# Kernel tuning notes

Measured on AMD Instinct MI355X. Metric: run time of the kernel, lower is better.

Reference implementation:

```python
import jax, jax.numpy as jnp
import numpy as np

V, E, H, T = 8000, 256, 256, 4  # vocab, embed, lstm hidden, tagset (BMES)
B, S = 64, 512


def setup_inputs() -> dict:
    key = jax.random.key(0)
    ks = jax.random.split(key, 16)
    w = lambda k, shape, s=0.05: (jax.random.normal(k, shape, jnp.float32) * s)
    return {
        "sentence": jax.random.randint(ks[0], (B, S), 0, V),
        "tags": jax.random.randint(ks[1], (B, S), 0, T),
        "length_list": jnp.full((B,), S, dtype=jnp.int32),
        "emb": w(ks[2], (V, E), 0.1),
        "Wih_f": w(ks[3], (4 * H, E)), "Whh_f": w(ks[4], (4 * H, H)), "b_f": jnp.zeros((4 * H,), jnp.float32),
        "Wih_b": w(ks[5], (4 * H, E)), "Whh_b": w(ks[6], (4 * H, H)), "b_b": jnp.zeros((4 * H,), jnp.float32),
        "Wlin": w(ks[7], (T, 2 * H), 0.05), "blin": jnp.zeros((T,), jnp.float32),
        "start_trans": w(ks[8], (T,), 0.1), "end_trans": w(ks[9], (T,), 0.1),
        "transitions": w(ks[10], (T, T), 0.1),
    }


def _lstm_dir(xs, Wih, Whh, b, reverse):
    # xs: [S, B, E] time-major; PyTorch gate order i,f,g,o
    Bv, Hh = xs.shape[1], Whh.shape[1]
    def step(carry, x):
        h, c = carry
        g = x @ Wih.T + h @ Whh.T + b
        i, f, gg, o = jnp.split(g, 4, axis=-1)
        c = jax.nn.sigmoid(f) * c + jax.nn.sigmoid(i) * jnp.tanh(gg)
        h = jax.nn.sigmoid(o) * jnp.tanh(c)
        return (h, c), h
    init = (jnp.zeros((Bv, Hh), xs.dtype), jnp.zeros((Bv, Hh), xs.dtype))
    _, hs = jax.lax.scan(step, init, xs, reverse=reverse)
    return hs  # [S, B, H]


def _crf_llh(emis, tagsT, start, end, trans):
    # emis: [S, B, T] time-major; tagsT: [S, B]. No mask (matches original call).
    e_sc = jnp.take_along_axis(emis, tagsT[:, :, None], axis=2)[..., 0]  # [S, B]
    tr_sc = trans[tagsT[:-1], tagsT[1:]]                                  # [S-1, B]
    num = start[tagsT[0]] + e_sc.sum(0) + tr_sc.sum(0) + end[tagsT[-1]]   # [B]
    alpha = start[None, :] + emis[0]                                      # [B, T]
    def step(alpha, e):
        return jax.nn.logsumexp(alpha[:, :, None] + trans[None], axis=1) + e, None
    alpha, _ = jax.lax.scan(step, alpha, emis[1:])
    denom = jax.nn.logsumexp(alpha + end[None, :], axis=1)                # [B]
    return num - denom


def _viterbi(emis, start, end, trans):
    # emis: [S, B, T] -> best tag path [B, S]
    score = start[None, :] + emis[0]                                      # [B, T]
    def step(score, e):
        cand = score[:, :, None] + trans[None]                            # [B, T_prev, T_next]
        bp = jnp.argmax(cand, axis=1)                                     # [B, T]
        return jnp.max(cand, axis=1) + e, bp
    score, bps = jax.lax.scan(step, score, emis[1:])                      # bps: [S-1, B, T]
    last = jnp.argmax(score + end[None, :], axis=1)                       # [B]
    def back(tag, bp):
        prev = jnp.take_along_axis(bp, tag[:, None], axis=1)[:, 0]
        return prev, prev
    _, path = jax.lax.scan(back, last, bps, reverse=True)                 # [S-1, B]
    return jnp.concatenate([path, last[None]], axis=0).T                  # [B, S]


def reference(sentence, tags, length_list, emb, Wih_f, Whh_f, b_f,
              Wih_b, Whh_b, b_b, Wlin, blin, start_trans, end_trans, transitions):
    xs = jnp.swapaxes(emb[sentence], 0, 1)                                # [S, B, E]
    hf = _lstm_dir(xs, Wih_f, Whh_f, b_f, reverse=False)
    hb = _lstm_dir(xs, Wih_b, Whh_b, b_b, reverse=True)
    h = jnp.concatenate([hf, hb], axis=-1)                                # [S, B, 2H] (dropout = eval identity)
    emis = h @ Wlin.T + blin                                              # [S, B, T]
    loss = -jnp.sum(_crf_llh(emis, tags.T, start_trans, end_trans, transitions))
    tag_seq = _viterbi(emis, start_trans, end_trans, transitions)
    return tag_seq, loss
```

## Files before the change

### kernel.cpp

```cpp
#include <hip/hip_runtime.h>
#include <math.h>

#define Vv 8000
#define Ee 256
#define Hh 256
#define Tt 4
#define Bb 64
#define Ss 512

#define EPROJ_PER_DIR (Vv * 1024)
#define WMAT_PER_DIR  (Ee * 1024)

#define NSTAT 8
#define NSTRM 24
#define STAT_U32 (NSTAT * 512 * 4)

#if defined(__has_builtin)
# if __has_builtin(__builtin_amdgcn_sdot4)
#  define HAS_SDOT4 1
# endif
# if __has_builtin(__builtin_amdgcn_exp2f) && __has_builtin(__builtin_amdgcn_rcpf)
#  define HAS_FASTTRANS 1
# endif
#endif

__device__ __forceinline__ float sigm(float x) { return 1.f / (1.f + expf(-x)); }

__device__ __forceinline__ float sigm_f(float x) {
#ifdef HAS_FASTTRANS
    const float e = __builtin_amdgcn_exp2f(-1.44269504f * x);
    return __builtin_amdgcn_rcpf(1.f + e);
#else
    return 1.f / (1.f + expf(-x));
#endif
}
__device__ __forceinline__ float tanh_f(float x) {
#ifdef HAS_FASTTRANS
    const float e = __builtin_amdgcn_exp2f(-2.88539008f * x);
    return 2.f * __builtin_amdgcn_rcpf(1.f + e) - 1.f;
#else
    return tanhf(x);
#endif
}

__device__ __forceinline__ int dot4i8(unsigned a, unsigned b, int c) {
#ifdef HAS_SDOT4
    return __builtin_amdgcn_sdot4((int)a, (int)b, c, false);
#else
    int s = c;
    #pragma unroll
    for (int i = 0; i < 4; ++i) {
        const int xa = ((int)(a << (24 - 8 * i))) >> 24;
        const int xb = ((int)(b << (24 - 8 * i))) >> 24;
        s += xa * xb;
    }
    return s;
#endif
}

__global__ void prep1_kernel(const float* __restrict__ Wih_f, const float* __restrict__ b_f,
                             const float* __restrict__ Wih_b, const float* __restrict__ b_b,
                             const float* __restrict__ Wlin,
                             float* __restrict__ WihP, float* __restrict__ bP,
                             float* __restrict__ WlinQ)
{
    int tid = blockIdx.x * blockDim.x + threadIdx.x;
    int dir = tid >> 18;
    int r   = tid & 262143;
    int k   = r >> 10;
    int jp  = r & 1023;
    int u   = jp >> 2;
    int g   = jp & 3;
    int row = g * 256 + u;
    const float* Wih = dir ? Wih_b : Wih_f;
    const float* bv  = dir ? b_b   : b_f;
    WihP[dir * WMAT_PER_DIR + k * 1024 + jp] = Wih[row * 256 + k];
    if (r < 1024) {
        bP[dir * 1024 + jp] = bv[row];
        int uu = r >> 2, tt = r & 3;
        WlinQ[(dir * 256 + uu) * 4 + tt] = Wlin[tt * (2 * Hh) + dir * 256 + uu];
    }
}

__global__ __launch_bounds__(256) void scale_kernel(const float* __restrict__ Whh_f,
                                                    const float* __restrict__ Whh_b,
                                                    float* __restrict__ scales)
{
    const int gw = blockIdx.x * 4 + (threadIdx.x >> 6);
    const int lane = threadIdx.x & 63;
    const int dir = gw >> 10;
    const int row = gw & 1023;
    const float* W = dir ? Whh_b : Whh_f;
    const float* src = W + (size_t)row * 256 + lane * 4;
    float m = fmaxf(fmaxf(fabsf(src[0]), fabsf(src[1])),
                    fmaxf(fabsf(src[2]), fabsf(src[3])));
    #pragma unroll
    for (int off = 32; off > 0; off >>= 1) m = fmaxf(m, __shfl_down(m, off));
    if (lane == 0) scales[gw] = fmaxf(m, 1e-12f) / 127.f;
}

__global__ __launch_bounds__(256) void quant_kernel(const float* __restrict__ Whh_f,
                                                    const float* __restrict__ Whh_b,
                                                    const float* __restrict__ scales,
                                                    unsigned int* __restrict__ W8)
{
    const int idx = blockIdx.x * 256 + threadIdx.x;
    const int dir = idx >> 16;
    const int rem = idx & 65535;
    int slot, t, j, kw;
    if (rem < STAT_U32) {
        slot = rem >> 11; const int r2 = rem & 2047; t = r2 >> 2; j = r2 & 3;
        kw = 2 * slot + (j >> 1);
    } else {
        const int q2 = rem - STAT_U32;
        slot = q2 >> 11; const int r2 = q2 & 2047; t = r2 >> 2; j = r2 & 3;
        kw = 2 * NSTAT + 2 * slot + (j >> 1);
    }
    const int rr = j & 1;
    const int u  = t >> 1;
    const int gs = (t & 1) * 2 + rr;
    const int row = gs * 256 + u;
    const float* W = dir ? Whh_b : Whh_f;
    const float sc = scales[dir * 1024 + row];
    const float inv = 1.f / sc;
    unsigned int v = 0;
    #pragma unroll
    for (int i = 0; i < 4; ++i) {
        const float w = W[(size_t)row * 256 + kw * 4 + i];
        int q = (int)rintf(w * inv);
        q = q > 127 ? 127 : (q < -127 ? -127 : q);
        v |= ((unsigned int)(unsigned char)(signed char)q) << (8 * i);
    }
    W8[idx] = v;
}

__global__ __launch_bounds__(512) void wl8_kernel(const float* __restrict__ Wlin,
                                                  unsigned int* __restrict__ wl8T,
                                                  float* __restrict__ scfac)
{
    const int w = threadIdx.x >> 6;
    const int lane = threadIdx.x & 63;
    const int dir = w >> 2, t = w & 3;
    const float4 v = *(const float4*)(Wlin + t * (2 * Hh) + dir * 256 + lane * 4);
    float m = fmaxf(fmaxf(fabsf(v.x), fabsf(v.y)), fmaxf(fabsf(v.z), fabsf(v.w)));
    #pragma unroll
    for (int off = 32; off > 0; off >>= 1) m = fmaxf(m, __shfl_down(m, off));
    const float mall = __builtin_amdgcn_readfirstlane(m);
    const float sc = fmaxf(mall, 1e-12f) / 127.f;
    const float inv = 1.f / sc;
    const float vv[4] = {v.x, v.y, v.z, v.w};
    unsigned int pk = 0;
    #pragma unroll
    for (int i = 0; i < 4; ++i) {
        int q = (int)rintf(vv[i] * inv);
        q = q > 127 ? 127 : (q < -127 ? -127 : q);
        pk |= ((unsigned int)(unsigned char)(signed char)q) << (8 * i);
    }
    wl8T[w * 64 + lane] = pk;
    if (lane == 0) scfac[w] = sc / 127.f;
}

#define BM 64
#define BN 128
#define BK 16
__global__ __launch_bounds__(256) void embproj_gemm(const float* __restrict__ emb,
                                                    const float* __restrict__ WihP,
                                                    const float* __restrict__ bP,
                                                    float* __restrict__ embproj)
{
    int dir = blockIdx.z;
    const float* Bmat = WihP + dir * WMAT_PER_DIR;
    float* C = embproj + (size_t)dir * EPROJ_PER_DIR;
    int m0 = blockIdx.x * BM;
    int n0 = blockIdx.y * BN;

    __shared__ float As[BK][BM];
    __shared__ float Bs[BK][BN];

    int t = threadIdx.x;
    int tm = (t & 15) * 4;
    int tn = (t >> 4) * 8;
    float acc[4][8];
    #pragma unroll
    for (int i = 0; i < 4; ++i)
        #pragma unroll
        for (int j = 0; j < 8; ++j) acc[i][j] = 0.f;

    for (int k0 = 0; k0 < Ee; k0 += BK) {
        {
            int row = t >> 2, seg = t & 3;
            float4 a4 = *(const float4*)(&emb[(size_t)(m0 + row) * Ee + k0 + seg * 4]);
            As[seg * 4 + 0][row] = a4.x;
            As[seg * 4 + 1][row] = a4.y;
            As[seg * 4 + 2][row] = a4.z;
            As[seg * 4 + 3][row] = a4.w;
        }
        {
            int kk = t >> 4, nn = (t & 15) * 8;
            float4 b0 = *(const float4*)(&Bmat[(size_t)(k0 + kk) * 1024 + n0 + nn]);
            float4 b1 = *(const float4*)(&Bmat[(size_t)(k0 + kk) * 1024 + n0 + nn + 4]);
            *(float4*)&Bs[kk][nn]     = b0;
            *(float4*)&Bs[kk][nn + 4] = b1;
        }
        __syncthreads();
        #pragma unroll
        for (int k = 0; k < BK; ++k) {
            float4 a  = *(const float4*)&As[k][tm];
            float4 b0 = *(const float4*)&Bs[k][tn];
            float4 b1 = *(const float4*)&Bs[k][tn + 4];
            float av[4] = {a.x, a.y, a.z, a.w};
            float bv[8] = {b0.x, b0.y, b0.z, b0.w, b1.x, b1.y, b1.z, b1.w};
            #pragma unroll
            for (int i = 0; i < 4; ++i)
                #pragma unroll
                for (int j = 0; j < 8; ++j)
                    acc[i][j] += av[i] * bv[j];
        }
        __syncthreads();
    }
    #pragma unroll
    for (int i = 0; i < 4; ++i) {
        int m = m0 + tm + i;
        #pragma unroll
        for (int j = 0; j < 8; j += 4) {
            float4 o;
            o.x = acc[i][j + 0] + bP[dir * 1024 + n0 + tn + j + 0];
            o.y = acc[i][j + 1] + bP[dir * 1024 + n0 + tn + j + 1];
            o.z = acc[i][j + 2] + bP[dir * 1024 + n0 + tn + j + 2];
            o.w = acc[i][j + 3] + bP[dir * 1024 + n0 + tn + j + 3];
            *(float4*)&C[(size_t)m * 1024 + n0 + tn + j] = o;
        }
    }
}

__global__ __attribute__((amdgpu_flat_work_group_size(512, 512)))
__attribute__((amdgpu_waves_per_eu(2, 2))) void lstm_stream_kernel(
    const int* __restrict__ sentence,
    const float* __restrict__ embproj,
    const unsigned int* __restrict__ W8,
    const float* __restrict__ scales,
    const unsigned int* __restrict__ wl8T,
    const float* __restrict__ scfac,
    float* __restrict__ emisP)
{
    extern __shared__ char smem[];
    uint4*        SWl = (uint4*)smem;
    unsigned int* h8  = (unsigned int*)(smem + STAT_U32*4);

    const int bx  = blockIdx.x;
    const int dir = bx >> 6;
    const int b   = bx & 63;
    const int t   = threadIdx.x;
    const int lane = t & 63, wv = t >> 6;
    const int u    = t >> 1;
    const int gs0  = (t & 1) * 2;
    const bool ev  = !(t & 1);

    const unsigned int* Wd   = W8 + (size_t)dir * 65536;
    const unsigned int* Wstr = Wd + STAT_U32;

    #pragma unroll
    for (int i = 0; i < NSTAT; ++i)
        SWl[i * 512 + t] = *(const uint4*)(Wd + (size_t)(i * 512 + t) * 4);
    if (t < 128) h8[t] = 0u;

    const float sc0 = scales[dir * 1024 + (gs0 + 0) * 256 + u] * (1.f / 127.f);
    const float sc1 = scales[dir * 1024 + (gs0 + 1) * 256 + u] * (1.f / 127.f);
    const float* EP = embproj + (size_t)dir * EPROJ_PER_DIR;
    const int* sent = sentence + (size_t)b * Ss;
    float c = 0.f;

    unsigned int wlq = 0;
    float efac = 0.f;
    const int etag = wv - 4;
    if (wv >= 4) {
        wlq  = wl8T[(dir * 4 + etag) * 64 + lane];
        efac = scfac[dir * 4 + etag];
    }

    float2 ep_cur;
    {
        const int pos0 = dir ? (Ss - 1) : 0;
        ep_cur = *(const float2*)(EP + (size_t)sent[pos0] * 1024 + u * 4 + gs0);
    }

    __syncthreads();

    for (int s = 0; s < Ss; ++s) {
        float2 ep_nxt = make_float2(0.f, 0.f);
        if (s + 1 < Ss) {
            const int pn = dir ? (Ss - 2 - s) : (s + 1);
            ep_nxt = *(const float2*)(EP + (size_t)sent[pn] * 1024 + u * 4 + gs0);
        }

        const int rp = (s + 1) & 1;
        const int wp = s & 1;
        const int v_h = (int)h8[rp * 64 + lane];

        uint4 sb[NSTRM];
        #pragma unroll
        for (int i = 0; i < NSTRM; ++i)
            sb[i] = *(const uint4*)(Wstr + (size_t)(i * 512 + t) * 4);

        if (wv >= 4 && s > 0) {
            int e = dot4i8(wlq, (unsigned)v_h, 0);
            #pragma unroll
            for (int off = 32; off > 0; off >>= 1) e += __shfl_down(e, off);
            if (lane == 0) {
                const int pp = dir ? (Ss - s) : (s - 1);
                emisP[(((size_t)dir * Ss + pp) * Bb + b) * 4 + etag] = (float)e * efac;
            }
        }

        int a0c[4] = {0, 0, 0, 0};
        int a1c[4] = {0, 0, 0, 0};
        #pragma unroll
        for (int i = 0; i < NSTAT; ++i) {
            const uint4 w = SWl[i * 512 + t];
            const unsigned h0 = (unsigned)__builtin_amdgcn_readlane(v_h, 2 * i);
            const unsigned h1 = (unsigned)__builtin_amdgcn_readlane(v_h, 2 * i + 1);
            const int q = i & 3;
            a0c[q] = dot4i8(w.x, h0, a0c[q]); a1c[q] = dot4i8(w.y, h0, a1c[q]);
            a0c[q] = dot4i8(w.z, h1, a0c[q]); a1c[q] = dot4i8(w.w, h1, a1c[q]);
        }
        #pragma unroll
        for (int i = 0; i < NSTRM; ++i) {
            const uint4 w = sb[i];
            const unsigned h0 = (unsigned)__builtin_amdgcn_readlane(v_h, 2 * NSTAT + 2 * i);
            const unsigned h1 = (unsigned)__builtin_amdgcn_readlane(v_h, 2 * NSTAT + 2 * i + 1);
            const int q = i & 3;
            a0c[q] = dot4i8(w.x, h0, a0c[q]); a1c[q] = dot4i8(w.y, h0, a1c[q]);
            a0c[q] = dot4i8(w.z, h1, a0c[q]); a1c[q] = dot4i8(w.w, h1, a1c[q]);
        }
        const int a0 = (a0c[0] + a0c[1]) + (a0c[2] + a0c[3]);
        const int a1 = (a1c[0] + a1c[1]) + (a1c[2] + a1c[3]);

        const float g0 = (float)a0 * sc0 + ep_cur.x;
        const float g1 = (float)a1 * sc1 + ep_cur.y;
        const float pg0 = __shfl_xor(g0, 1);
        const float pg1 = __shfl_xor(g1, 1);
        if (ev) {
            c = sigm_f(g1) * c + sigm_f(g0) * tanh_f(pg0);
            const float h = sigm_f(pg1) * tanh_f(c);
            ((char*)h8)[wp * 256 + u] = (char)(int)rintf(h * 127.f);
        }
        ep_cur = ep_nxt;
        __syncthreads();
    }

    if (wv >= 4) {
        const int v_h = (int)h8[((Ss - 1) & 1) * 64 + lane];
        int e = dot4i8(wlq, (unsigned)v_h, 0);
        #pragma unroll
        for (int off = 32; off > 0; off >>= 1) e += __shfl_down(e, off);
        if (lane == 0) {
            const int pp = dir ? 0 : (Ss - 1);
            emisP[(((size_t)dir * Ss + pp) * Bb + b) * 4 + etag] = (float)e * efac;
        }
    }
}

#define EM2(S_, B_, J_) (emisA[(((size_t)(S_)) * Bb + (B_)) * 4 + (J_)] + \
                         emisB[(((size_t)(S_)) * Bb + (B_)) * 4 + (J_)])

__global__ __launch_bounds__(64) void tail_kernel(
    const float* __restrict__ emisA, const float* __restrict__ emisB,
    const float* __restrict__ blin, const float* __restrict__ start_t,
    const float* __restrict__ end_t, const float* __restrict__ trans,
    const int* __restrict__ tags, float* __restrict__ out_tags,
    float* __restrict__ out_loss)
{
    const int blk = blockIdx.x;
    const int t = threadIdx.x;
    const int b_loc = t >> 2, j = t & 3;
    const int base = t & ~3;

    if (blk < 4) {
        __shared__ unsigned char bp_sh[16][513][4];
        __shared__ unsigned char tag_sh[16][520];
        const int b = blk * 16 + b_loc;
        const float trj0 = trans[0*4+j], trj1 = trans[1*4+j],
                    trj2 = trans[2*4+j], trj3 = trans[3*4+j];
        const float blj = blin[j];
        float score = start_t[j] + EM2(0, b, j) + blj;
        for (int s = 1; s < Ss; ++s) {
            const float e = EM2(s, b, j) + blj;
            const float s0 = __shfl(score, base+0), s1 = __shfl(score, base+1),
                        s2 = __shfl(score, base+2), s3 = __shfl(score, base+3);
            float best = s0 + trj0; int bi = 0;
            float v = s1 + trj1; if (v > best) { best = v; bi = 1; }
            v = s2 + trj2; if (v > best) { best = v; bi = 2; }
            v = s3 + trj3; if (v > best) { best = v; bi = 3; }
            score = best + e;
            bp_sh[b_loc][s][j] = (unsigned char)bi;
        }
        const float fv = score + end_t[j];
        const float f0 = __shfl(fv, base+0), f1 = __shfl(fv, base+1),
                    f2 = __shfl(fv, base+2), f3 = __shfl(fv, base+3);
        __syncthreads();
        if (j == 0) {
            float best = f0; int tag = 0;
            if (f1 > best) { best = f1; tag = 1; }
            if (f2 > best) { best = f2; tag = 2; }
            if (f3 > best) { best = f3; tag = 3; }
            tag_sh[b_loc][Ss-1] = (unsigned char)tag;
            for (int s = Ss - 1; s >= 1; --s) {
                tag = bp_sh[b_loc][s][tag];
                tag_sh[b_loc][s-1] = (unsigned char)tag;
            }
        }
        __syncthreads();
        for (int idx = t; idx < 16 * Ss; idx += 64) {
            const int bl = idx >> 9, s = idx & (Ss - 1);
            out_tags[(size_t)(blk*16 + bl) * Ss + s] = (float)tag_sh[bl][s];
        }
    } else {
        const int b = (blk - 4) * 16 + b_loc;
        const float trj0 = trans[0*4+j], trj1 = trans[1*4+j],
                    trj2 = trans[2*4+j], trj3 = trans[3*4+j];
        const float blj = blin[j];
        float alpha = start_t[j] + EM2(0, b, j) + blj;
        for (int s = 1; s < Ss; ++s) {
            const float e = EM2(s, b, j) + blj;
            const float a0 = __shfl(alpha, base+0), a1 = __shfl(alpha, base+1),
                        a2 = __shfl(alpha, base+2), a3 = __shfl(alpha, base+3);
            const float x0 = a0 + trj0, x1 = a1 + trj1, x2 = a2 + trj2, x3 = a3 + trj3;
            const float m = fmaxf(fmaxf(x0, x1), fmaxf(x2, x3));
            alpha = m + logf(expf(x0-m) + expf(x1-m) + expf(x2-m) + expf(x3-m)) + e;
        }
        const float dv = alpha + end_t[j];
        const float d0 = __shfl(dv, base+0), d1 = __shfl(dv, base+1),
                    d2 = __shfl(dv, base+2), d3 = __shfl(dv, base+3);
        const float dm = fmaxf(fmaxf(d0, d1), fmaxf(d2, d3));
        const float denom = dm + logf(expf(d0-dm) + expf(d1-dm) + expf(d2-dm) + expf(d3-dm));

        const int lo = j * 128, hi = lo + 128;
        float num = 0.f;
        int tprev = (lo > 0) ? tags[(size_t)b*Ss + lo - 1] : 0;
        if (j == 0) num += start_t[tags[(size_t)b*Ss]];
        if (j == 3) num += end_t[tags[(size_t)b*Ss + Ss - 1]];
        for (int s = lo; s < hi; ++s) {
            const int tg = tags[(size_t)b*Ss + s];
            num += EM2(s, b, tg) + blin[tg];
            if (s > 0) num += trans[tprev*4 + tg];
            tprev = tg;
        }
        num += __shfl_xor(num, 1);
        num += __shfl_xor(num, 2);
        float lb = (j == 0) ? (denom - num) : 0.f;
        #pragma unroll
        for (int off = 32; off > 0; off >>= 1) lb += __shfl_down(lb, off);
        if (t == 0) atomicAdd(out_loss, lb);
    }
}

extern "C" void kernel_launch(void* const* d_in, const int* in_sizes, int n_in,
                              void* d_out, int out_size, void* d_ws, size_t ws_size,
                              hipStream_t stream)
{
    const int*   sentence = (const int*)d_in[0];
    const int*   tags     = (const int*)d_in[1];
    const float* emb      = (const float*)d_in[3];
    const float* Wih_f    = (const float*)d_in[4];
    const float* Whh_f    = (const float*)d_in[5];
    const float* b_f      = (const float*)d_in[6];
    const float* Wih_b    = (const float*)d_in[7];
    const float* Whh_b    = (const float*)d_in[8];
    const float* b_b      = (const float*)d_in[9];
    const float* Wlin     = (const float*)d_in[10];
    const float* blin     = (const float*)d_in[11];
    const float* start_t  = (const float*)d_in[12];
    const float* end_t    = (const float*)d_in[13];
    const float* trans    = (const float*)d_in[14];

    float*        embproj = (float*)d_ws;
    float*        WihP    = embproj + 2 * EPROJ_PER_DIR;
    float*        bP      = WihP + 2 * WMAT_PER_DIR;
    float*        WlinQ   = bP + 2048;
    float*        scales  = WlinQ + 2048;
    unsigned int* W8      = (unsigned int*)(scales + 2048);
    unsigned int* wl8T    = W8 + 131072;
    float*        scfac   = (float*)(wl8T + 512);
    float*        emisP   = scfac + 56;
    float*        emisA   = emisP;
    float*        emisB   = emisP + Ss * Bb * 4;

    prep1_kernel<<<2048, 256, 0, stream>>>(Wih_f, b_f, Wih_b, b_b, Wlin,
                                           WihP, bP, WlinQ);
    scale_kernel<<<512, 256, 0, stream>>>(Whh_f, Whh_b, scales);
    quant_kernel<<<512, 256, 0, stream>>>(Whh_f, Whh_b, scales, W8);
    wl8_kernel<<<1, 512, 0, stream>>>(Wlin, wl8T, scfac);

    dim3 gg(Vv / BM, 1024 / BN, 2);
    embproj_gemm<<<gg, 256, 0, stream>>>(emb, WihP, bP, embproj);

    lstm_stream_kernel<<<128, 512, STAT_U32 * 4 + 512, stream>>>(
        sentence, embproj, W8, scales, wl8T, scfac, emisP);

    float* out = (float*)d_out;
    float* out_loss = out + Bb * Ss;
    hipMemsetAsync(out_loss, 0, sizeof(float), stream);
    tail_kernel<<<8, 64, 0, stream>>>(emisA, emisB, blin, start_t, end_t, trans,
                                      tags, out, out_loss);
}
```

Before: 901.5 us.

## Split LSTM recurrent dot product over K halves with 1024-thread blocks

```diff
diff --git a/kernel.cpp b/kernel.cpp
--- a/kernel.cpp
+++ b/kernel.cpp
@@ -11,9 +11,9 @@
 #define EPROJ_PER_DIR (Vv * 1024)
 #define WMAT_PER_DIR  (Ee * 1024)
 
-#define NSTAT 8
-#define NSTRM 24
-#define STAT_U32 (NSTAT * 512 * 4)
+#define NSTAT 4
+#define NSTRM 12
+#define STAT_U32 (NSTAT * 1024 * 4)
 
 #if defined(__has_builtin)
 # if __has_builtin(__builtin_amdgcn_sdot4)
@@ -107,18 +107,20 @@
     const int idx = blockIdx.x * 256 + threadIdx.x;
     const int dir = idx >> 16;
     const int rem = idx & 65535;
-    int slot, t, j, kw;
+    int slot, t, j, kwoff;
     if (rem < STAT_U32) {
-        slot = rem >> 11; const int r2 = rem & 2047; t = r2 >> 2; j = r2 & 3;
-        kw = 2 * slot + (j >> 1);
+        slot = rem >> 12; const int r2 = rem & 4095; t = r2 >> 2; j = r2 & 3;
+        kwoff = 2 * slot + (j >> 1);
     } else {
         const int q2 = rem - STAT_U32;
-        slot = q2 >> 11; const int r2 = q2 & 2047; t = r2 >> 2; j = r2 & 3;
-        kw = 2 * NSTAT + 2 * slot + (j >> 1);
-    }
+        slot = q2 >> 12; const int r2 = q2 & 4095; t = r2 >> 2; j = r2 & 3;
+        kwoff = 2 * NSTAT + 2 * slot + (j >> 1);
+    }
+    const int kw = 32 * (t >> 9) + kwoff;
     const int rr = j & 1;
-    const int u  = t >> 1;
-    const int gs = (t & 1) * 2 + rr;
+    const int tt = t & 511;
+    const int u  = tt >> 1;
+    const int gs = (tt & 1) * 2 + rr;
     const int row = gs * 256 + u;
     const float* W = dir ? Whh_b : Whh_f;
     const float sc = scales[dir * 1024 + row];
@@ -233,8 +235,8 @@
     }
 }
 
-__global__ __attribute__((amdgpu_flat_work_group_size(512, 512)))
-__attribute__((amdgpu_waves_per_eu(2, 2))) void lstm_stream_kernel(
+__global__ __attribute__((amdgpu_flat_work_group_size(1024, 1024)))
+__attribute__((amdgpu_waves_per_eu(4, 4))) void lstm_stream_kernel(
     const int* __restrict__ sentence,
     const float* __restrict__ embproj,
     const unsigned int* __restrict__ W8,
@@ -244,24 +246,28 @@
     float* __restrict__ emisP)
 {
     extern __shared__ char smem[];
-    uint4*        SWl = (uint4*)smem;
-    unsigned int* h8  = (unsigned int*)(smem + STAT_U32*4);
+    uint4*        SWl  = (uint4*)smem;
+    unsigned int* h8   = (unsigned int*)(smem + STAT_U32*4);
+    int2*         part = (int2*)(smem + STAT_U32*4 + 512);
 
     const int bx  = blockIdx.x;
     const int dir = bx >> 6;
     const int b   = bx & 63;
     const int t   = threadIdx.x;
     const int lane = t & 63, wv = t >> 6;
-    const int u    = t >> 1;
-    const int gs0  = (t & 1) * 2;
-    const bool ev  = !(t & 1);
+    const int kh  = t >> 9;
+    const int tt  = t & 511;
+    const int u    = tt >> 1;
+    const int gs0  = (tt & 1) * 2;
+    const bool ev  = !(tt & 1);
+    const int kwb  = 32 * kh;
 
     const unsigned int* Wd   = W8 + (size_t)dir * 65536;
     const unsigned int* Wstr = Wd + STAT_U32;
 
     #pragma unroll
     for (int i = 0; i < NSTAT; ++i)
-        SWl[i * 512 + t] = *(const uint4*)(Wd + (size_t)(i * 512 + t) * 4);
+        SWl[i * 1024 + t] = *(const uint4*)(Wd + (size_t)(i * 1024 + t) * 4);
     if (t < 128) h8[t] = 0u;
 
     const float sc0 = scales[dir * 1024 + (gs0 + 0) * 256 + u] * (1.f / 127.f);
@@ -273,13 +279,13 @@
     unsigned int wlq = 0;
     float efac = 0.f;
     const int etag = wv - 4;
-    if (wv >= 4) {
+    if (wv >= 4 && wv < 8) {
         wlq  = wl8T[(dir * 4 + etag) * 64 + lane];
         efac = scfac[dir * 4 + etag];
     }
 
-    float2 ep_cur;
-    {
+    float2 ep_cur = make_float2(0.f, 0.f);
+    if (kh == 0) {
         const int pos0 = dir ? (Ss - 1) : 0;
         ep_cur = *(const float2*)(EP + (size_t)sent[pos0] * 1024 + u * 4 + gs0);
     }
@@ -288,7 +294,7 @@
 
     for (int s = 0; s < Ss; ++s) {
         float2 ep_nxt = make_float2(0.f, 0.f);
-        if (s + 1 < Ss) {
+        if (kh == 0 && s + 1 < Ss) {
             const int pn = dir ? (Ss - 2 - s) : (s + 1);
             ep_nxt = *(const float2*)(EP + (size_t)sent[pn] * 1024 + u * 4 + gs0);
         }
@@ -300,9 +306,9 @@
         uint4 sb[NSTRM];
         #pragma unroll
         for (int i = 0; i < NSTRM; ++i)
-            sb[i] = *(const uint4*)(Wstr + (size_t)(i * 512 + t) * 4);
-
-        if (wv >= 4 && s > 0) {
+            sb[i] = *(const uint4*)(Wstr + (size_t)(i * 1024 + t) * 4);
+
+        if (wv >= 4 && wv < 8 && s > 0) {
             int e = dot4i8(wlq, (unsigned)v_h, 0);
             #pragma unroll
             for (int off = 32; off > 0; off >>= 1) e += __shfl_down(e, off);
@@ -316,9 +322,9 @@
         int a1c[4] = {0, 0, 0, 0};
         #pragma unroll
         for (int i = 0; i < NSTAT; ++i) {
-            const uint4 w = SWl[i * 512 + t];
-            const unsigned h0 = (unsigned)__builtin_amdgcn_readlane(v_h, 2 * i);
-            const unsigned h1 = (unsigned)__builtin_amdgcn_readlane(v_h, 2 * i + 1);
+            const uint4 w = SWl[i * 1024 + t];
+            const unsigned h0 = (unsigned)__builtin_amdgcn_readlane(v_h, kwb + 2 * i);
+            const unsigned h1 = (unsigned)__builtin_amdgcn_readlane(v_h, kwb + 2 * i + 1);
             const int q = i & 3;
             a0c[q] = dot4i8(w.x, h0, a0c[q]); a1c[q] = dot4i8(w.y, h0, a1c[q]);
             a0c[q] = dot4i8(w.z, h1, a0c[q]); a1c[q] = dot4i8(w.w, h1, a1c[q]);
@@ -326,8 +332,8 @@
         #pragma unroll
         for (int i = 0; i < NSTRM; ++i) {
             const uint4 w = sb[i];
-            const unsigned h0 = (unsigned)__builtin_amdgcn_readlane(v_h, 2 * NSTAT + 2 * i);
-            const unsigned h1 = (unsigned)__builtin_amdgcn_readlane(v_h, 2 * NSTAT + 2 * i + 1);
+            const unsigned h0 = (unsigned)__builtin_amdgcn_readlane(v_h, kwb + 2 * NSTAT + 2 * i);
+            const unsigned h1 = (unsigned)__builtin_amdgcn_readlane(v_h, kwb + 2 * NSTAT + 2 * i + 1);
             const int q = i & 3;
             a0c[q] = dot4i8(w.x, h0, a0c[q]); a1c[q] = dot4i8(w.y, h0, a1c[q]);
             a0c[q] = dot4i8(w.z, h1, a0c[q]); a1c[q] = dot4i8(w.w, h1, a1c[q]);
@@ -335,20 +341,26 @@
         const int a0 = (a0c[0] + a0c[1]) + (a0c[2] + a0c[3]);
         const int a1 = (a1c[0] + a1c[1]) + (a1c[2] + a1c[3]);
 
-        const float g0 = (float)a0 * sc0 + ep_cur.x;
-        const float g1 = (float)a1 * sc1 + ep_cur.y;
-        const float pg0 = __shfl_xor(g0, 1);
-        const float pg1 = __shfl_xor(g1, 1);
-        if (ev) {
-            c = sigm_f(g1) * c + sigm_f(g0) * tanh_f(pg0);
-            const float h = sigm_f(pg1) * tanh_f(c);
-            ((char*)h8)[wp * 256 + u] = (char)(int)rintf(h * 127.f);
+        if (kh == 1) part[tt] = make_int2(a0, a1);
+        __syncthreads();
+
+        if (kh == 0) {
+            const int2 p = part[tt];
+            const float g0 = (float)(a0 + p.x) * sc0 + ep_cur.x;
+            const float g1 = (float)(a1 + p.y) * sc1 + ep_cur.y;
+            const float pg0 = __shfl_xor(g0, 1);
+            const float pg1 = __shfl_xor(g1, 1);
+            if (ev) {
+                c = sigm_f(g1) * c + sigm_f(g0) * tanh_f(pg0);
+                const float h = sigm_f(pg1) * tanh_f(c);
+                ((char*)h8)[wp * 256 + u] = (char)(int)rintf(h * 127.f);
+            }
         }
         ep_cur = ep_nxt;
         __syncthreads();
     }
 
-    if (wv >= 4) {
+    if (wv >= 4 && wv < 8) {
         const int v_h = (int)h8[((Ss - 1) & 1) * 64 + lane];
         int e = dot4i8(wlq, (unsigned)v_h, 0);
         #pragma unroll
@@ -494,7 +506,7 @@
     dim3 gg(Vv / BM, 1024 / BN, 2);
     embproj_gemm<<<gg, 256, 0, stream>>>(emb, WihP, bP, embproj);
 
-    lstm_stream_kernel<<<128, 512, STAT_U32 * 4 + 512, stream>>>(
+    lstm_stream_kernel<<<128, 1024, STAT_U32 * 4 + 512 + 4096, stream>>>(
         sentence, embproj, W8, scales, wl8T, scfac, emisP);
 
     float* out = (float*)d_out;
```

Measured after the change: 1.159 ms. 1.29x slower.
